# Optimization experiments

Measured on AMD Instinct MI355X. Metric: run time of the kernel, lower is better.

## Reference

```python
import jax, jax.numpy as jnp
import numpy as np

N_RAYS = 1_048_576
T_ITERS = 4
N_POINTS = 8
DIM = 64
N_LAYERS = 2
INF = 1e9


def setup_inputs() -> dict:
    key = jax.random.key(0)
    ks = jax.random.split(key, 12)
    orig = jax.random.normal(ks[0], (N_RAYS, 3), jnp.float32)
    vec = jax.random.normal(ks[1], (N_RAYS, 3), jnp.float32)
    masks = jax.random.bernoulli(ks[2], 0.6, (T_ITERS, N_RAYS))
    bbox_idxs = jax.random.randint(ks[3], (T_ITERS, N_RAYS), 0, 1024, jnp.int32)
    t1 = jax.random.uniform(ks[4], (T_ITERS, N_RAYS), jnp.float32) * 2.0
    t2 = t1 + jax.random.uniform(ks[5], (T_ITERS, N_RAYS), jnp.float32) * 2.0
    mesh_min = jnp.array([-1.0, -1.0, -1.0], jnp.float32)
    mesh_max = jnp.array([1.0, 1.0, 1.0], jnp.float32)
    s = 0.05
    W0 = jax.random.normal(ks[6], (3 * N_POINTS, DIM), jnp.float32) * s
    b0 = jnp.zeros((DIM,), jnp.float32)
    ln_g = jnp.ones((N_LAYERS, DIM), jnp.float32)
    ln_b = jnp.zeros((N_LAYERS, DIM), jnp.float32)
    Ws = jax.random.normal(ks[7], (N_LAYERS, DIM, DIM), jnp.float32) * s
    bs = jnp.zeros((N_LAYERS, DIM), jnp.float32)
    Wc = jax.random.normal(ks[8], (DIM,), jnp.float32) * s
    bc = jnp.zeros((), jnp.float32)
    Wd = jax.random.normal(ks[9], (DIM,), jnp.float32) * s
    bd = jnp.zeros((), jnp.float32)
    return dict(orig=orig, vec=vec, masks=masks, bbox_idxs=bbox_idxs, t1=t1, t2=t2,
                mesh_min=mesh_min, mesh_max=mesh_max, W0=W0, b0=b0,
                ln_g=ln_g, ln_b=ln_b, Ws=Ws, bs=bs, Wc=Wc, bc=bc, Wd=Wd, bd=bd)


def _layernorm(x, g, b):
    mu = jnp.mean(x, axis=-1, keepdims=True)
    var = jnp.mean((x - mu) ** 2, axis=-1, keepdims=True)
    return (x - mu) * jax.lax.rsqrt(var + 1e-5) * g + b


def _net_forward(x, W0, b0, ln_g, ln_b, Ws, bs, Wc, bc, Wd, bd):
    # x: [N, 3*n_points]
    y = x @ W0 + b0
    for i in range(N_LAYERS):
        y = jax.nn.relu(y)
        y = _layernorm(y, ln_g[i], ln_b[i])
        y = y @ Ws[i] + bs[i]
    y = jax.nn.relu(y)
    cls = y @ Wc + bc   # [N]
    dist = y @ Wd + bd  # [N]
    return cls, dist


def reference(orig, vec, masks, bbox_idxs, t1, t2, mesh_min, mesh_max,
              W0, b0, ln_g, ln_b, Ws, bs, Wc, bc, Wd, bd):
    n_rays = orig.shape[0]
    ts = jnp.linspace(0.0, 1.0, N_POINTS, dtype=jnp.float32)
    min_infl = mesh_min - 0.5 * (mesh_max - mesh_min)
    max_infl = mesh_max + 0.5 * (mesh_max - mesh_min)
    scale = max_infl - min_infl
    dist = jnp.full((n_rays,), INF, jnp.float32)
    for it in range(T_ITERS):
        mask, ct1, ct2 = masks[it], t1[it], t2[it]
        inp_orig = orig + vec * ct1[:, None]          # [N,3]
        inp_vec = vec * (ct2 - ct1)[:, None]          # [N,3]
        # sample n_points along segment: [N, P, 3]
        inp = inp_orig[:, None, :] + inp_vec[:, None, :] * ts[None, :, None]
        inp = (inp - min_infl) / scale
        x = inp.reshape(n_rays, -1)                   # [N, 3P]
        hit_c, dv_c = _net_forward(x, W0, b0, ln_g, ln_b, Ws, bs, Wc, bc, Wd, bd)
        hit = jnp.where(mask, hit_c, 0.0)             # masked_scatter_ equivalent
        dv = jnp.where(mask, dv_c, 0.0) + ct1
        upd = (hit > 0) & (dv < dist) & mask
        dist = jnp.where(upd, dv, dist)
    dist = jnp.where(dist == INF, 0.0, dist)
    return (dist > 0, dist)
```

## Files before the change

kernel.cpp:

```cpp
#include <hip/hip_runtime.h>
#include <hip/hip_bf16.h>
#include <stdint.h>

#define NRAYS 1048576
#define INFV  1e9f
#define TBIG  1e30f

typedef short short8 __attribute__((ext_vector_type(8)));
typedef float f32x4  __attribute__((ext_vector_type(4)));

#define WS_B0   16
#define FB0     1024
#define FB1     2048

#define PKLO(a,b) ((int)(((unsigned)(a) & 0xFFFFu) | ((unsigned)(b) << 16)))
#define PKHI(a,b) ((int)(((unsigned)(a) >> 16) | ((unsigned)(b) & 0xFFFF0000u)))

__device__ __forceinline__ int pklo(int a, int b) {
    return (int)__builtin_amdgcn_perm((unsigned)b, (unsigned)a, 0x05040100u);
}
__device__ __forceinline__ int pkhi(int a, int b) {
    return (int)__builtin_amdgcn_perm((unsigned)b, (unsigned)a, 0x07060302u);
}

__device__ __forceinline__ float ldf(const void* p, int i, int fm) {
    if (fm) return ((const float*)p)[i];
    unsigned u = ((const unsigned short*)p)[i];
    return __uint_as_float(u << 16);
}

__device__ __forceinline__ void split3(float f, int& him, int& lo_raw) {
    unsigned u = __float_as_uint(f);
    float r = f - __uint_as_float(u & 0xFFFF0000u);
    unsigned um = __float_as_uint(r);
    float r2 = r - __uint_as_float(um & 0xFFFF0000u);
    him    = pkhi((int)u, (int)um);
    lo_raw = (int)__float_as_uint(r2);
}

__device__ __forceinline__ unsigned comp16(int h, float f) {
    unsigned u = __float_as_uint(f);
    if (h == 0) return u >> 16;
    float r = f - __uint_as_float(u & 0xFFFF0000u);
    unsigned um = __float_as_uint(r);
    if (h == 1) return um >> 16;
    float r2 = r - __uint_as_float(um & 0xFFFF0000u);
    return __float_as_uint(r2) >> 16;
}

__device__ __forceinline__ float rsum16(float x) {
    int v;
    v = __builtin_amdgcn_update_dpp(0, __float_as_int(x), 0x128, 0xF, 0xF, false); x += __int_as_float(v);
    v = __builtin_amdgcn_update_dpp(0, __float_as_int(x), 0x124, 0xF, 0xF, false); x += __int_as_float(v);
    v = __builtin_amdgcn_update_dpp(0, __float_as_int(x), 0x122, 0xF, 0xF, false); x += __int_as_float(v);
    v = __builtin_amdgcn_update_dpp(0, __float_as_int(x), 0x121, 0xF, 0xF, false); x += __int_as_float(v);
    return x;
}

union I4S8 { int4 i; short8 s; };
__device__ __forceinline__ short8 mk8i(int a, int b, int c, int d) {
    I4S8 u; u.i = make_int4(a, b, c, d); return u.s;
}
__device__ __forceinline__ short8 ld_frag(const unsigned* p) {
    I4S8 u; u.i = *(const int4*)p; return u.s;
}

__global__ __launch_bounds__(256) void conv_k(
    const void* __restrict__ mmin, const void* __restrict__ mmax,
    const void* __restrict__ masks,
    const void* __restrict__ W0, const void* __restrict__ b0,
    const void* __restrict__ lng, const void* __restrict__ lnb,
    const void* __restrict__ Ws, const void* __restrict__ bs,
    const void* __restrict__ Wc, const void* __restrict__ bc,
    const void* __restrict__ Wd, const void* __restrict__ bd,
    unsigned* __restrict__ ws)
{
    __shared__ int sfm;
    float* wf = (float*)ws;
    const int tid = threadIdx.x;
    if (tid == 0) {
        unsigned w0 = ((const unsigned*)mmin)[0];
        int fm = ((w0 & 0xFFFFu) == 0u) ? 1 : 0;
        const unsigned* mw = (const unsigned*)masks;
        bool sawBf = false, allBin = true, sawF32 = false;
        for (int i = 0; i < 64; ++i) {
            unsigned w = mw[i], lo = w & 0xFFFFu, hi = w >> 16;
            if (lo == 0x3F80u && (hi == 0x3F80u || hi == 0u)) sawBf = true;
            if (w == 0x3F800000u) sawF32 = true;
            if (w > 1u) allBin = false;
        }
        int ms = sawBf ? 2 : (allBin ? 4 : (sawF32 ? 4 : 1));
        ws[8] = (unsigned)fm; ws[9] = (unsigned)ms;
        for (int c = 0; c < 3; ++c) {
            float mn = ldf(mmin, c, fm), mx = ldf(mmax, c, fm);
            float ext = mx - mn;
            wf[c]     = mn - 0.5f * ext;
            wf[3 + c] = 1.0f / (2.0f * ext);
        }
        wf[6] = ldf(bc, 0, fm);
        wf[7] = ldf(bd, 0, fm);
        sfm = fm;
    }
    __syncthreads();
    const int fm = sfm;

    for (int i = tid; i < 64;  i += 256) { wf[16 + i] = ldf(b0, i, fm); wf[464 + i] = ldf(Wc, i, fm); wf[528 + i] = ldf(Wd, i, fm); }
    for (int i = tid; i < 128; i += 256) { wf[80 + i] = ldf(bs, i, fm); wf[208 + i] = ldf(lng, i, fm); wf[336 + i] = ldf(lnb, i, fm); }

    for (int w = tid; w < 768; w += 256) {
        int ct = w / 192, rem = w % 192;
        int h = rem / 64, wi = rem % 64;
        int lane16 = wi >> 2, p = wi & 3;
        int n = ct * 16 + lane16;
        unsigned word = 0;
        #pragma unroll
        for (int half = 0; half < 2; ++half) {
            int k = 2 * p + half;
            float v = 0.f;
            if (k < 3) {
                for (int pp = 0; pp < 8; ++pp) v += ldf(W0, (3 * pp + k) * 64 + n, fm);
            } else if (k < 6) {
                int c3 = k - 3;
                for (int pp = 0; pp < 8; ++pp) v = fmaf((float)((double)pp / 7.0), ldf(W0, (3 * pp + c3) * 64 + n, fm), v);
            }
            word |= comp16(h, v) << (16 * half);
        }
        ws[FB0 + ((ct * 3 + h) * 16 + lane16) * 4 + p] = word;
    }

    for (int w = tid; w < 12288; w += 256) {
        int li = w / 6144, inner = w % 6144;
        int t = inner >> 8;
        int h = t % 3, ckc = t / 3, kc = ckc & 1, ct = ckc >> 1;
        int wi = inner & 255, lane = wi >> 2, p = wi & 3;
        int qq = lane >> 4, cc = lane & 15;
        int n = ct * 16 + cc;
        int k0 = kc * 32 + qq * 8 + 2 * p;
        float f0 = ldf(Ws, li * 4096 + k0 * 64 + n, fm);
        float f1 = ldf(Ws, li * 4096 + (k0 + 1) * 64 + n, fm);
        ws[FB1 + w] = comp16(h, f0) | (comp16(h, f1) << 16);
    }
}

#define ST1_S 34
#define ST2_S 34

__global__ __launch_bounds__(64, 4) void nbvh_main(
    const void* __restrict__ orig_p, const void* __restrict__ vec_p,
    const void* __restrict__ masks_p, const void* __restrict__ t1_p,
    const void* __restrict__ t2_p, const unsigned* __restrict__ wsu,
    void* __restrict__ out_p)
{
    __shared__ __align__(16) unsigned sT1[16][ST1_S];
    __shared__ __align__(16) unsigned sT2[16][ST2_S];
    __shared__ float sOV[6][64];
    __shared__ float sT1m[4][64];
    __shared__ float sT2g[4][64];
    __shared__ float sB[448];
    __shared__ float sDf[64];

    const float* wf = (const float*)wsu;
    const int fm = (int)wsu[8];
    const int ms = (int)wsu[9];
    const float bcv = wf[6], bdv = wf[7];

    const int L = threadIdx.x;
    const int q = L >> 4, c = L & 15;
    const int ray = blockIdx.x * 64 + L;

    for (int i = L; i < 448; i += 64) sB[i] = wf[16 + i];

    {
        const float mn0 = wf[0], mn1 = wf[1], mn2 = wf[2];
        const float is0 = wf[3], is1 = wf[4], is2 = wf[5];
        const float o0 = ldf(orig_p, 3*ray+0, fm), o1 = ldf(orig_p, 3*ray+1, fm), o2 = ldf(orig_p, 3*ray+2, fm);
        const float v0 = ldf(vec_p,  3*ray+0, fm), v1 = ldf(vec_p,  3*ray+1, fm), v2 = ldf(vec_p,  3*ray+2, fm);
        sOV[0][L] = (o0 - mn0) * is0;  sOV[1][L] = (o1 - mn1) * is1;  sOV[2][L] = (o2 - mn2) * is2;
        sOV[3][L] = v0 * is0;          sOV[4][L] = v1 * is1;          sOV[5][L] = v2 * is2;
        #pragma unroll
        for (int it = 0; it < 4; ++it) {
            const int gi = it * NRAYS + ray;
            bool mk;
            if      (ms == 1) mk = ((const uint8_t*) masks_p)[gi] != 0;
            else if (ms == 2) mk = ((const uint16_t*)masks_p)[gi] != 0;
            else              mk = ((const unsigned*) masks_p)[gi] != 0;
            sT1m[it][L] = mk ? ldf(t1_p, gi, fm) : TBIG;
            sT2g[it][L] = ldf(t2_p, gi, fm);
        }
        sDf[L] = INFV;
    }
    __syncthreads();

    #pragma unroll 1
    for (int rt = 0; rt < 4; ++rt) {
        #pragma unroll 1
        for (int ip = 0; ip < 2; ++ip) {
            f32x4 acc[2][4];
            short8 Ah[2][2], Am[2][2], Al[2][2];

            {
                short8 Xh[2], Xm[2], Xl[2];
                #pragma unroll
                for (int itl = 0; itl < 2; ++itl) {
                    const int it = ip * 2 + itl;
                    const int row = rt * 16 + c;
                    const float t1v = sT1m[it][row];
                    const float dtv = sT2g[it][row] - t1v;
                    float x[6];
                    #pragma unroll
                    for (int j = 0; j < 3; ++j) {
                        float ov = sOV[j][row], vv = sOV[3 + j][row];
                        x[j]     = fmaf(vv, t1v, ov);
                        x[3 + j] = vv * dtv;
                    }
                    int him[6], lo[6];
                    #pragma unroll
                    for (int j = 0; j < 6; ++j) split3(q == 0 ? x[j] : 0.f, him[j], lo[j]);
                    Xh[itl] = mk8i(pklo(him[0],him[1]), pklo(him[2],him[3]), pklo(him[4],him[5]), 0);
                    Xm[itl] = mk8i(pkhi(him[0],him[1]), pkhi(him[2],him[3]), pkhi(him[4],him[5]), 0);
                    Xl[itl] = mk8i(pkhi(lo[0], lo[1]),  pkhi(lo[2], lo[3]),  pkhi(lo[4], lo[5]),  0);
                }
                #pragma unroll
                for (int itl = 0; itl < 2; ++itl)
                    #pragma unroll
                    for (int ct = 0; ct < 4; ++ct) {
                        float b = sB[ct * 16 + c];
                        f32x4 a; a[0]=a[1]=a[2]=a[3]=b; acc[itl][ct]=a;
                    }
                __builtin_amdgcn_s_setprio(1);
                #pragma unroll
                for (int ct = 0; ct < 4; ++ct) {
                    short8 Bh = (q==0) ? ld_frag(wsu + FB0 + ((ct*3+0)*16 + c)*4) : mk8i(0,0,0,0);
                    short8 Bm = (q==0) ? ld_frag(wsu + FB0 + ((ct*3+1)*16 + c)*4) : mk8i(0,0,0,0);
                    short8 Bl = (q==0) ? ld_frag(wsu + FB0 + ((ct*3+2)*16 + c)*4) : mk8i(0,0,0,0);
                    #pragma unroll
                    for (int itl = 0; itl < 2; ++itl) {
                        acc[itl][ct] = __builtin_amdgcn_mfma_f32_16x16x32_bf16(Xh[itl], Bh, acc[itl][ct], 0,0,0);
                        acc[itl][ct] = __builtin_amdgcn_mfma_f32_16x16x32_bf16(Xh[itl], Bm, acc[itl][ct], 0,0,0);
                        acc[itl][ct] = __builtin_amdgcn_mfma_f32_16x16x32_bf16(Xm[itl], Bh, acc[itl][ct], 0,0,0);
                        acc[itl][ct] = __builtin_amdgcn_mfma_f32_16x16x32_bf16(Xm[itl], Bm, acc[itl][ct], 0,0,0);
                        acc[itl][ct] = __builtin_amdgcn_mfma_f32_16x16x32_bf16(Xh[itl], Bl, acc[itl][ct], 0,0,0);
                        acc[itl][ct] = __builtin_amdgcn_mfma_f32_16x16x32_bf16(Xl[itl], Bh, acc[itl][ct], 0,0,0);
                    }
                }
                __builtin_amdgcn_s_setprio(0);
            }

            #pragma unroll 1
            for (int layer = 0; layer < 2; ++layer) {
                const unsigned* fb = wsu + FB1 + layer * 6144;
                const int bo = 64 + layer * 64, go = 192 + layer * 64, ho = 320 + layer * 64;

                #pragma unroll
                for (int itl = 0; itl < 2; ++itl) {
                    __syncthreads();
                    float z[4][4];
                    #pragma unroll
                    for (int ct = 0; ct < 4; ++ct)
                        #pragma unroll
                        for (int e = 0; e < 4; ++e) z[ct][e] = fmaxf(acc[itl][ct][e], 0.f);
                    float mu[4], rs[4];
                    #pragma unroll
                    for (int e = 0; e < 4; ++e) {
                        float s  = z[0][e] + z[1][e] + z[2][e] + z[3][e];
                        float s2 = fmaf(z[0][e], z[0][e], fmaf(z[1][e], z[1][e],
                                   fmaf(z[2][e], z[2][e], z[3][e] * z[3][e])));
                        s  = rsum16(s);
                        s2 = rsum16(s2);
                        mu[e] = s * (1.0f / 64.0f);
                        float var = fmaf(-mu[e], mu[e], s2 * (1.0f / 64.0f));
                        rs[e] = rsqrtf(var + 1e-5f);
                    }
                    int him[4][4], lov[4][4];
                    #pragma unroll
                    for (int ct = 0; ct < 4; ++ct) {
                        const float gv = sB[go + ct * 16 + c];
                        const float hv = sB[ho + ct * 16 + c];
                        #pragma unroll
                        for (int e = 0; e < 4; ++e) {
                            float y = fmaf((z[ct][e] - mu[e]) * rs[e], gv, hv);
                            split3(y, him[ct][e], lov[ct][e]);
                        }
                    }
                    #pragma unroll
                    for (int e = 0; e < 4; ++e) {
                        const int row = q * 4 + e;
                        sT1[row][c]      = (unsigned)him[0][e];
                        sT1[row][c + 16] = (unsigned)him[1][e];
                        sT2[row][c]      = (unsigned)pkhi(lov[0][e], lov[2][e]);
                        sT2[row][c + 16] = (unsigned)pkhi(lov[1][e], lov[3][e]);
                    }
                    __syncthreads();
                    const int4 t01 = *(const int4*)&sT2[c][q*8];
                    const int4 t23 = *(const int4*)&sT2[c][q*8 + 4];
                    {
                        const int4 w01 = *(const int4*)&sT1[c][q*8];
                        const int4 w23 = *(const int4*)&sT1[c][q*8 + 4];
                        Ah[itl][0] = mk8i(pklo(w01.x,w01.y), pklo(w01.z,w01.w), pklo(w23.x,w23.y), pklo(w23.z,w23.w));
                        Am[itl][0] = mk8i(pkhi(w01.x,w01.y), pkhi(w01.z,w01.w), pkhi(w23.x,w23.y), pkhi(w23.z,w23.w));
                        Al[itl][0] = mk8i(pklo(t01.x,t01.y), pklo(t01.z,t01.w), pklo(t23.x,t23.y), pklo(t23.z,t23.w));
                    }
                    __syncthreads();
                    #pragma unroll
                    for (int e = 0; e < 4; ++e) {
                        const int row = q * 4 + e;
                        sT1[row][c]      = (unsigned)him[2][e];
                        sT1[row][c + 16] = (unsigned)him[3][e];
                    }
                    __syncthreads();
                    {
                        const int4 w01 = *(const int4*)&sT1[c][q*8];
                        const int4 w23 = *(const int4*)&sT1[c][q*8 + 4];
                        Ah[itl][1] = mk8i(pklo(w01.x,w01.y), pklo(w01.z,w01.w), pklo(w23.x,w23.y), pklo(w23.z,w23.w));
                        Am[itl][1] = mk8i(pkhi(w01.x,w01.y), pkhi(w01.z,w01.w), pkhi(w23.x,w23.y), pkhi(w23.z,w23.w));
                        Al[itl][1] = mk8i(pkhi(t01.x,t01.y), pkhi(t01.z,t01.w), pkhi(t23.x,t23.y), pkhi(t23.z,t23.w));
                    }
                }

                #pragma unroll
                for (int itl = 0; itl < 2; ++itl)
                    #pragma unroll
                    for (int ct = 0; ct < 4; ++ct) {
                        float b = sB[bo + ct * 16 + c];
                        f32x4 a; a[0]=a[1]=a[2]=a[3]=b; acc[itl][ct]=a;
                    }
                __builtin_amdgcn_s_setprio(1);
                #pragma unroll
                for (int kc = 0; kc < 2; ++kc) {
                    #pragma unroll
                    for (int ct = 0; ct < 4; ++ct) {
                        short8 Bh = ld_frag(fb + (((ct*2+kc)*3 + 0) << 8) + (L << 2));
                        short8 Bm = ld_frag(fb + (((ct*2+kc)*3 + 1) << 8) + (L << 2));
                        short8 Bl = ld_frag(fb + (((ct*2+kc)*3 + 2) << 8) + (L << 2));
                        #pragma unroll
                        for (int itl = 0; itl < 2; ++itl) {
                            acc[itl][ct] = __builtin_amdgcn_mfma_f32_16x16x32_bf16(Ah[itl][kc], Bh, acc[itl][ct], 0,0,0);
                            acc[itl][ct] = __builtin_amdgcn_mfma_f32_16x16x32_bf16(Ah[itl][kc], Bm, acc[itl][ct], 0,0,0);
                            acc[itl][ct] = __builtin_amdgcn_mfma_f32_16x16x32_bf16(Am[itl][kc], Bh, acc[itl][ct], 0,0,0);
                            acc[itl][ct] = __builtin_amdgcn_mfma_f32_16x16x32_bf16(Am[itl][kc], Bm, acc[itl][ct], 0,0,0);
                            acc[itl][ct] = __builtin_amdgcn_mfma_f32_16x16x32_bf16(Ah[itl][kc], Bl, acc[itl][ct], 0,0,0);
                            acc[itl][ct] = __builtin_amdgcn_mfma_f32_16x16x32_bf16(Al[itl][kc], Bh, acc[itl][ct], 0,0,0);
                        }
                    }
                }
                __builtin_amdgcn_s_setprio(0);
            }

            {
                float wcr[4], wdr[4];
                #pragma unroll
                for (int ct = 0; ct < 4; ++ct) {
                    wcr[ct] = wf[464 + ct * 16 + c];
                    wdr[ct] = wf[528 + ct * 16 + c];
                }
                #pragma unroll
                for (int e = 0; e < 4; ++e) {
                    const int idx = rt * 16 + q * 4 + e;
                    float d = sDf[idx];
                    #pragma unroll
                    for (int itl = 0; itl < 2; ++itl) {
                        const int it = ip * 2 + itl;
                        float cp = 0.f, dp = 0.f;
                        #pragma unroll
                        for (int ct = 0; ct < 4; ++ct) {
                            float f = fmaxf(acc[itl][ct][e], 0.f);
                            cp = fmaf(f, wcr[ct], cp);
                            dp = fmaf(f, wdr[ct], dp);
                        }
                        cp = rsum16(cp); dp = rsum16(dp);
                        float cls = cp + bcv;
                        float dv  = dp + bdv + sT1m[it][idx];
                        if (cls > 0.f && dv < d) d = dv;
                    }
                    if (c == 0) sDf[idx] = d;
                }
            }
        }
    }

    __syncthreads();
    float d = sDf[L];
    if (d == INFV) d = 0.f;
    const float hit = (d > 0.f) ? 1.f : 0.f;
    if (fm) {
        ((float*)out_p)[ray]         = hit;
        ((float*)out_p)[NRAYS + ray] = d;
    } else {
        __hip_bfloat16* o = (__hip_bfloat16*)out_p;
        o[ray]         = __float2bfloat16(hit);
        o[NRAYS + ray] = __float2bfloat16(d);
    }
}

extern "C" void kernel_launch(void* const* d_in, const int* in_sizes, int n_in,
                              void* d_out, int out_size, void* d_ws, size_t ws_size,
                              hipStream_t stream) {
    (void)in_sizes; (void)n_in; (void)ws_size; (void)out_size;
    unsigned* ws = (unsigned*)d_ws;
    conv_k<<<1, 256, 0, stream>>>(
        d_in[6], d_in[7], d_in[2],
        d_in[8], d_in[9], d_in[10], d_in[11],
        d_in[12], d_in[13], d_in[14], d_in[15],
        d_in[16], d_in[17], ws);
    nbvh_main<<<NRAYS / 64, 64, 0, stream>>>(
        d_in[0], d_in[1], d_in[2], d_in[4], d_in[5], ws, d_out);
}
```

Baseline: 711.8 us.

## Fold LayerNorm affine into next-layer weights and replace barriers with waitcnt

```diff
diff --git a/kernel.cpp b/kernel.cpp
--- a/kernel.cpp
+++ b/kernel.cpp
@@ -64,6 +64,8 @@
 __device__ __forceinline__ short8 ld_frag(const unsigned* p) {
     I4S8 u; u.i = *(const int4*)p; return u.s;
 }
+
+#define WSYNC() asm volatile("s_waitcnt lgkmcnt(0)" ::: "memory")
 
 __global__ __launch_bounds__(256) void conv_k(
     const void* __restrict__ mmin, const void* __restrict__ mmax,
@@ -105,7 +107,13 @@
     const int fm = sfm;
 
     for (int i = tid; i < 64;  i += 256) { wf[16 + i] = ldf(b0, i, fm); wf[464 + i] = ldf(Wc, i, fm); wf[528 + i] = ldf(Wd, i, fm); }
-    for (int i = tid; i < 128; i += 256) { wf[80 + i] = ldf(bs, i, fm); wf[208 + i] = ldf(lng, i, fm); wf[336 + i] = ldf(lnb, i, fm); }
+    for (int i = tid; i < 128; i += 256) {
+        int li = i >> 6, n = i & 63;
+        float b = ldf(bs, i, fm);
+        for (int k = 0; k < 64; ++k)
+            b = fmaf(ldf(lnb, li * 64 + k, fm), ldf(Ws, li * 4096 + k * 64 + n, fm), b);
+        wf[80 + i] = b;
+    }
 
     for (int w = tid; w < 768; w += 256) {
         int ct = w / 192, rem = w % 192;
@@ -136,8 +144,10 @@
         int qq = lane >> 4, cc = lane & 15;
         int n = ct * 16 + cc;
         int k0 = kc * 32 + qq * 8 + 2 * p;
-        float f0 = ldf(Ws, li * 4096 + k0 * 64 + n, fm);
-        float f1 = ldf(Ws, li * 4096 + (k0 + 1) * 64 + n, fm);
+        float g0 = ldf(lng, li * 64 + k0, fm);
+        float g1 = ldf(lng, li * 64 + k0 + 1, fm);
+        float f0 = g0 * ldf(Ws, li * 4096 + k0 * 64 + n, fm);
+        float f1 = g1 * ldf(Ws, li * 4096 + (k0 + 1) * 64 + n, fm);
         ws[FB1 + w] = comp16(h, f0) | (comp16(h, f1) << 16);
     }
 }
@@ -156,7 +166,7 @@
     __shared__ float sOV[6][64];
     __shared__ float sT1m[4][64];
     __shared__ float sT2g[4][64];
-    __shared__ float sB[448];
+    __shared__ float sB[192];
     __shared__ float sDf[64];
 
     const float* wf = (const float*)wsu;
@@ -168,7 +178,7 @@
     const int q = L >> 4, c = L & 15;
     const int ray = blockIdx.x * 64 + L;
 
-    for (int i = L; i < 448; i += 64) sB[i] = wf[16 + i];
+    for (int i = L; i < 192; i += 64) sB[i] = wf[16 + i];
 
     {
         const float mn0 = wf[0], mn1 = wf[1], mn2 = wf[2];
@@ -189,7 +199,7 @@
         }
         sDf[L] = INFV;
     }
-    __syncthreads();
+    WSYNC();
 
     #pragma unroll 1
     for (int rt = 0; rt < 4; ++rt) {
@@ -215,7 +225,7 @@
                     }
                     int him[6], lo[6];
                     #pragma unroll
-                    for (int j = 0; j < 6; ++j) split3(q == 0 ? x[j] : 0.f, him[j], lo[j]);
+                    for (int j = 0; j < 6; ++j) split3(x[j], him[j], lo[j]);
                     Xh[itl] = mk8i(pklo(him[0],him[1]), pklo(him[2],him[3]), pklo(him[4],him[5]), 0);
                     Xm[itl] = mk8i(pkhi(him[0],him[1]), pkhi(him[2],him[3]), pkhi(him[4],him[5]), 0);
                     Xl[itl] = mk8i(pkhi(lo[0], lo[1]),  pkhi(lo[2], lo[3]),  pkhi(lo[4], lo[5]),  0);
@@ -249,11 +259,11 @@
             #pragma unroll 1
             for (int layer = 0; layer < 2; ++layer) {
                 const unsigned* fb = wsu + FB1 + layer * 6144;
-                const int bo = 64 + layer * 64, go = 192 + layer * 64, ho = 320 + layer * 64;
+                const int bo = 64 + layer * 64;
 
                 #pragma unroll
                 for (int itl = 0; itl < 2; ++itl) {
-                    __syncthreads();
+                    WSYNC();
                     float z[4][4];
                     #pragma unroll
                     for (int ct = 0; ct < 4; ++ct)
@@ -274,11 +284,9 @@
                     int him[4][4], lov[4][4];
                     #pragma unroll
                     for (int ct = 0; ct < 4; ++ct) {
-                        const float gv = sB[go + ct * 16 + c];
-                        const float hv = sB[ho + ct * 16 + c];
                         #pragma unroll
                         for (int e = 0; e < 4; ++e) {
-                            float y = fmaf((z[ct][e] - mu[e]) * rs[e], gv, hv);
+                            float y = (z[ct][e] - mu[e]) * rs[e];
                             split3(y, him[ct][e], lov[ct][e]);
                         }
                     }
@@ -290,7 +298,7 @@
                         sT2[row][c]      = (unsigned)pkhi(lov[0][e], lov[2][e]);
                         sT2[row][c + 16] = (unsigned)pkhi(lov[1][e], lov[3][e]);
                     }
-                    __syncthreads();
+                    WSYNC();
                     const int4 t01 = *(const int4*)&sT2[c][q*8];
                     const int4 t23 = *(const int4*)&sT2[c][q*8 + 4];
                     {
@@ -300,14 +308,14 @@
                         Am[itl][0] = mk8i(pkhi(w01.x,w01.y), pkhi(w01.z,w01.w), pkhi(w23.x,w23.y), pkhi(w23.z,w23.w));
                         Al[itl][0] = mk8i(pklo(t01.x,t01.y), pklo(t01.z,t01.w), pklo(t23.x,t23.y), pklo(t23.z,t23.w));
                     }
-                    __syncthreads();
+                    WSYNC();
                     #pragma unroll
                     for (int e = 0; e < 4; ++e) {
                         const int row = q * 4 + e;
                         sT1[row][c]      = (unsigned)him[2][e];
                         sT1[row][c + 16] = (unsigned)him[3][e];
                     }
-                    __syncthreads();
+                    WSYNC();
                     {
                         const int4 w01 = *(const int4*)&sT1[c][q*8];
                         const int4 w23 = *(const int4*)&sT1[c][q*8 + 4];
@@ -378,7 +386,7 @@
         }
     }
 
-    __syncthreads();
+    WSYNC();
     float d = sDf[L];
     if (d == INFV) d = 0.f;
     const float hit = (d > 0.f) ? 1.f : 0.f;
```

Result: no change. 707.2 us (median of 2 runs) (-0.6%).
